# Kernel tuning notes

Hardware: AMD Instinct MI355X
Metric: run time of the kernel (lower is better)

Reference implementation:

```python
import jax, jax.numpy as jnp
import numpy as np

H, W, NUM_HEADS = 32, 32, 8


def dwconv3x3(x, w, b):
    # x: (B,C,H,W), w: (C,1,3,3) depthwise, b: (C,)
    y = jax.lax.conv_general_dilated(
        x, w, window_strides=(1, 1), padding='SAME',
        dimension_numbers=('NCHW', 'OIHW', 'NCHW'),
        feature_group_count=x.shape[1])
    return y + b[None, :, None, None]


def conv1x1(x, w, b):
    # x: (B,C,H,W), w: (O,C), b: (O,)
    return jnp.einsum('oc,bchw->bohw', w, x) + b[None, :, None, None]


def layernorm(x, w, b, eps=1e-6):
    mu = x.mean(-1, keepdims=True)
    var = ((x - mu) ** 2).mean(-1, keepdims=True)
    return (x - mu) / jnp.sqrt(var + eps) * w + b


def setup_inputs() -> dict:
    key = jax.random.key(0)
    ks = jax.random.split(key, 12)
    B, N, C = 32, H * W, 512
    Ch = 4 * C  # inverted MLP hidden
    s_lin = 0.02
    s_dw = np.sqrt(2.0 / 9.0)   # fan_out init for 3x3 depthwise
    s_pw1 = np.sqrt(2.0 / Ch)
    s_pw2 = np.sqrt(2.0 / C)
    return {
        'x': jax.random.normal(ks[0], (B, N, C), jnp.float32),
        'cpe_w': jax.random.normal(ks[1], (C, 1, 3, 3), jnp.float32) * s_dw,
        'cpe_b': jnp.zeros((C,), jnp.float32),
        'ln1_w': jnp.ones((C,), jnp.float32),
        'ln1_b': jnp.zeros((C,), jnp.float32),
        'qkv_w': jax.random.normal(ks[2], (3 * C, C), jnp.float32) * s_lin,
        'crpe_w': jax.random.normal(ks[3], (C, 1, 3, 3), jnp.float32) * s_dw,
        'crpe_b': jnp.zeros((C,), jnp.float32),
        'ln2_w': jnp.ones((C,), jnp.float32),
        'ln2_b': jnp.zeros((C,), jnp.float32),
        'fc1_w': jax.random.normal(ks[4], (Ch, C), jnp.float32) * s_pw1,
        'fc1_b': jnp.zeros((Ch,), jnp.float32),
        'dw_w': jax.random.normal(ks[5], (Ch, 1, 3, 3), jnp.float32) * s_dw,
        'dw_b': jnp.zeros((Ch,), jnp.float32),
        'fc2_w': jax.random.normal(ks[6], (C, Ch), jnp.float32) * s_pw2,
        'fc2_b': jnp.zeros((C,), jnp.float32),
    }


def reference(x, cpe_w, cpe_b, ln1_w, ln1_b, qkv_w, crpe_w, crpe_b,
              ln2_w, ln2_b, fc1_w, fc1_b, dw_w, dw_b, fc2_w, fc2_b):
    B, N, C = x.shape
    h = NUM_HEADS
    d = C // h
    scale = d ** -0.5

    # --- Convolutional position encoding: x = x + dwconv(x) ---
    img = x.reshape(B, H, W, C).transpose(0, 3, 1, 2)  # B C H W
    img = img + dwconv3x3(img, cpe_w, cpe_b)
    x = img.transpose(0, 2, 3, 1).reshape(B, N, C)

    # --- Factorized attention + conv relative position encoding ---
    cur = layernorm(x, ln1_w, ln1_b)
    qkv = cur @ qkv_w.T                                 # (B,N,3C)
    qkv = qkv.reshape(B, N, 3, h, d).transpose(2, 0, 3, 1, 4)  # (3,B,h,N,d)
    q, k, v = qkv[0], qkv[1], qkv[2]
    k_softmax = jax.nn.softmax(k, axis=2)               # softmax over tokens N
    ktv = jnp.einsum('bhnk,bhnv->bhkv', k_softmax, v)   # (B,h,d,d)
    factor_att = jnp.einsum('bhnk,bhkv->bhnv', q, ktv)  # (B,h,N,d)
    # crpe: depthwise conv on v as image, elementwise-multiplied by q
    v_img = v.transpose(0, 1, 3, 2).reshape(B, h * d, H, W)
    v_img = dwconv3x3(v_img, crpe_w, crpe_b)
    v_conv = v_img.reshape(B, h, d, N).transpose(0, 1, 3, 2)
    crpe = q * v_conv
    attn_out = (scale * factor_att + crpe).transpose(0, 2, 1, 3).reshape(B, N, C)
    x = x + attn_out

    # --- Inverted MLP (conv-based channel mixing) ---
    cur = layernorm(x, ln2_w, ln2_b)
    img = cur.reshape(B, H, W, C).transpose(0, 3, 1, 2)  # B C H W
    hdn = conv1x1(img, fc1_w, fc1_b)
    hdn = jax.nn.gelu(hdn, approximate=False)
    hdn = hdn + dwconv3x3(hdn, dw_w, dw_b)
    out = conv1x1(hdn, fc2_w, fc2_b)
    x = x + out.transpose(0, 2, 3, 1).reshape(B, N, C)
    return x
```

## Files before the change

### kernel.cpp

```cpp
#include <hip/hip_runtime.h>
#include <hip/hip_bf16.h>

using bf16 = __hip_bfloat16;
using s16x4 = __attribute__((ext_vector_type(4))) short;
using s16x8 = __attribute__((ext_vector_type(8))) short;
using f32x4 = __attribute__((ext_vector_type(4))) float;

#define DI __device__ __forceinline__

template <int N> DI void wvm() {
    if constexpr (N == 8) asm volatile("s_waitcnt vmcnt(8)" ::: "memory");
    else if constexpr (N == 4) asm volatile("s_waitcnt vmcnt(4)" ::: "memory");
    else if constexpr (N == 2) asm volatile("s_waitcnt vmcnt(2)" ::: "memory");
    else asm volatile("s_waitcnt vmcnt(0)" ::: "memory");
}

DI float b2f(short s) { union { unsigned u; float f; } z; z.u = ((unsigned)(unsigned short)s) << 16; return z.f; }
DI short f2b(float f) { bf16 t = __float2bfloat16(f); return *(short*)&t; }

DI float gelu_f(float x) {
    const float t = 0.7978845608f * x * (1.f + 0.044715f * x * x);
    const float e = __expf(2.f * t);
    const float th = 1.f - 2.f / (e + 1.f);
    return 0.5f * x * (1.f + th);
}

DI void ld8(const bf16* p, float* f) {
    s16x8 x = *(const s16x8*)(const void*)p;
#pragma unroll
    for (int c = 0; c < 8; c++) f[c] = b2f(x[c]);
}
DI void ld8(const float* p, float* f) {
    float4 a = *(const float4*)p, b = *(const float4*)(p + 4);
    f[0]=a.x; f[1]=a.y; f[2]=a.z; f[3]=a.w; f[4]=b.x; f[5]=b.y; f[6]=b.z; f[7]=b.w;
}

typedef const __attribute__((address_space(1))) void* gp_t;
typedef __attribute__((address_space(3))) void* lp_t;
DI void gload_lds16(const void* g, void* l) {
    __builtin_amdgcn_global_load_lds((gp_t)g, (lp_t)l, 16, 0, 0);
}

__global__ void diag_k(float* out, float v) { out[0] = v; }

__global__ void f2bf_k(const float* __restrict__ in, bf16* __restrict__ out, int n) {
    int i = (blockIdx.x * 256 + threadIdx.x) * 8;
    if (i >= n) return;
    float f[8];
    ld8(in + i, f);
    s16x8 o;
#pragma unroll
    for (int c = 0; c < 8; c++) o[c] = f2b(f[c]);
    *(s16x8*)(void*)(out + i) = o;
}

DI void tap10(const float* r, float w0, float w1, float w2, float* acc) {
#pragma unroll
    for (int i = 0; i < 8; i++)
        acc[i] += w0 * r[i] + w1 * r[i + 1] + w2 * r[i + 2];
}

template <typename TI, typename TO, bool RESID, int CPL>
__global__ __launch_bounds__(256) void conv4_k(
    const TI* in, long rs, long coff,
    const float* __restrict__ w, const float* __restrict__ bias,
    TO* out, long ors, int gshift)
{
    constexpr int CH = 64 * CPL;
    constexpr int ECNT = CH / 8;
    __shared__ float buf[2][CH][33];
    const int t = threadIdx.x;
    const int band = blockIdx.x & 3;
    const int cg = (blockIdx.x >> 2) & ((1 << gshift) - 1);
    const int img = blockIdx.x >> (2 + gshift);
    const int y0 = band * 8;

    const int spx = t >> 3;
    const int sce = (t & 7) * ECNT;
    const TI* gsrc = in + ((long)img << 10) * rs + coff + (long)cg * CH + sce;

    const int c = t & 63;
    const int xb = (t >> 6) * 8;

    float wv9[9][CPL], bw[CPL];
#pragma unroll
    for (int p = 0; p < CPL; p++) {
        const int gch = cg * CH + c * CPL + p;
#pragma unroll
        for (int j = 0; j < 9; j++) wv9[j][p] = w[gch * 9 + j];
        bw[p] = bias[gch];
    }

    auto stage = [&](int row) {
        float f[ECNT];
        ld8(gsrc + (long)(row * 32 + spx) * rs, f);
        if constexpr (ECNT == 16) ld8(gsrc + (long)(row * 32 + spx) * rs + 8, f + 8);
        float* d = &buf[row & 1][0][0];
#pragma unroll
        for (int k = 0; k < ECNT; k++) {
            const int ch = sce + k;
            const int rr = (CPL == 2) ? ((ch & 1) * 64 + (ch >> 1)) : ch;
            d[rr * 33 + spx] = f[k];
        }
    };
    auto slice = [&](int row, float r[CPL][10]) {
#pragma unroll
        for (int p = 0; p < CPL; p++) {
            const float* s = &buf[row & 1][c + p * 64][0];
            r[p][0] = (xb == 0) ? 0.f : s[xb - 1];
#pragma unroll
            for (int i = 0; i < 8; i++) r[p][1 + i] = s[xb + i];
            r[p][9] = (xb + 8 >= 32) ? 0.f : s[xb + 8];
        }
    };
    auto zero = [&](float r[CPL][10]) {
#pragma unroll
        for (int p = 0; p < CPL; p++)
#pragma unroll
            for (int i = 0; i < 10; i++) r[p][i] = 0.f;
    };

    float r0[CPL][10], r1[CPL][10], r2[CPL][10];
    if (y0 > 0) stage(y0 - 1);
    __syncthreads();
    if (y0 > 0) slice(y0 - 1, r0); else zero(r0);
    stage(y0);
    __syncthreads();
    slice(y0, r1);

    for (int y = y0; y < y0 + 8; ++y) {
        const int yn = y + 1;
        if (yn <= 31) stage(yn);
        __syncthreads();
        if (yn <= 31) slice(yn, r2); else zero(r2);
        float acc[CPL][8];
#pragma unroll
        for (int p = 0; p < CPL; p++) {
#pragma unroll
            for (int i = 0; i < 8; i++) acc[p][i] = bw[p];
            tap10(r0[p], wv9[0][p], wv9[1][p], wv9[2][p], acc[p]);
            tap10(r1[p], wv9[3][p], wv9[4][p], wv9[5][p], acc[p]);
            tap10(r2[p], wv9[6][p], wv9[7][p], wv9[8][p], acc[p]);
            if (RESID) {
#pragma unroll
                for (int i = 0; i < 8; i++) acc[p][i] += r1[p][i + 1];
            }
        }
        TO* o = out + ((long)(img * 1024 + y * 32 + xb)) * ors + (long)cg * CH + c * CPL;
#pragma unroll
        for (int i = 0; i < 8; i++) {
            if constexpr (CPL == 2 && sizeof(TO) == 2) {
                const unsigned u = (unsigned)(unsigned short)f2b(acc[0][i]) |
                                   ((unsigned)(unsigned short)f2b(acc[1][i]) << 16);
                *(unsigned*)(void*)(o + (long)i * ors) = u;
            } else {
                o[(long)i * ors] = (TO)acc[0][i];
            }
        }
#pragma unroll
        for (int p = 0; p < CPL; p++)
#pragma unroll
            for (int i = 0; i < 10; i++) { r0[p][i] = r1[p][i]; r1[p][i] = r2[p][i]; }
    }
}

__global__ __launch_bounds__(256) void ln_k(const float* __restrict__ x,
                                            const float* __restrict__ w,
                                            const float* __restrict__ bp,
                                            bf16* __restrict__ out)
{
    const size_t row = blockIdx.x * 4 + (threadIdx.x >> 6);
    const int t = threadIdx.x & 63;
    const float* xr = x + row * 512;
    alignas(16) float v[8];
    *(float4*)&v[0] = *(const float4*)(xr + t * 8);
    *(float4*)&v[4] = *(const float4*)(xr + t * 8 + 4);
    float s = 0.f;
#pragma unroll
    for (int j = 0; j < 8; j++) s += v[j];
#pragma unroll
    for (int mm = 32; mm; mm >>= 1) s += __shfl_xor(s, mm);
    const float mu = s * (1.f / 512.f);
    float q = 0.f;
#pragma unroll
    for (int j = 0; j < 8; j++) { v[j] -= mu; q += v[j] * v[j]; }
#pragma unroll
    for (int mm = 32; mm; mm >>= 1) q += __shfl_xor(q, mm);
    const float rstd = rsqrtf(q * (1.f / 512.f) + 1e-6f);
    alignas(16) float wv[8], bv[8];
    *(float4*)&wv[0] = *(const float4*)(w + t * 8);
    *(float4*)&wv[4] = *(const float4*)(w + t * 8 + 4);
    *(float4*)&bv[0] = *(const float4*)(bp + t * 8);
    *(float4*)&bv[4] = *(const float4*)(bp + t * 8 + 4);
    alignas(16) bf16 o[8];
#pragma unroll
    for (int j = 0; j < 8; j++) o[j] = __float2bfloat16(v[j] * rstd * wv[j] + bv[j]);
    *(uint4*)(out + row * 512 + t * 8) = *(const uint4*)o;
}

template <int EPI, int K, int NY, bool DUAL = false>
__global__ __launch_bounds__(512) void gemm8p_k(
    const bf16* __restrict__ A, const bf16* __restrict__ A2,
    const bf16* __restrict__ Bw, const float* __restrict__ bias,
    const float* resid, bf16* __restrict__ outb, float* outf, int M, int Nn)
{
    constexpr int KT = K / 64;
    constexpr int LDA = DUAL ? K / 2 : K;
    __shared__ __align__(16) char lds[131072];
    char* ldsA = lds;
    char* ldsB = lds + 65536;
    const int t = threadIdx.x;
    const int lane = t & 63;
    const int w = t >> 6;
    const int wr = w >> 2, wc = w & 3;
    const int nwg = 128 * NY;
    const int swz = (blockIdx.x & 7) * (nwg >> 3) + (blockIdx.x >> 3);
    const int m0 = (swz / NY) * 256;
    const int n0 = (swz % NY) * 256;
    const int lr = lane & 15, lg = lane >> 4;

    f32x4 acc[8][4] = {};

    const int srow = lane >> 3;
    const int ssrc = 8 * ((lane & 7) ^ srow);

    auto SA = [&](int b, int kt, int h) {
        const bf16* Ab = A;
        int ktl = kt;
        if constexpr (DUAL) { if (kt >= KT / 2) { Ab = A2; ktl = kt - KT / 2; } }
#pragma unroll
        for (int j = 0; j < 2; j++) {
            const int lrow0 = j * 64 + w * 8;
            const int R0 = j * 128 + h * 64 + (lrow0 & 63);
            gload_lds16(Ab + (size_t)(m0 + R0 + srow) * LDA + ktl * 64 + ssrc,
                        ldsA + ((b * 2 + h) * 128 + lrow0) * 128);
        }
    };
    auto SB = [&](int b, int kt, int h) {
#pragma unroll
        for (int j = 0; j < 2; j++) {
            const int lrow0 = j * 64 + w * 8;
            const int R0 = (lrow0 >> 5) * 64 + h * 32 + (lrow0 & 31);
            gload_lds16(Bw + (size_t)(n0 + R0 + srow) * K + kt * 64 + ssrc,
                        ldsB + ((b * 2 + h) * 128 + lrow0) * 128);
        }
    };
    auto RA = [&](int b, int h, int m, int ks) -> s16x8 {
        return *(const s16x8*)(ldsA + ((b * 2 + h) * 128 + wr * 64 + m * 16 + lr) * 128
                               + (((ks * 4 + lg) ^ (lr & 7)) << 4));
    };
    auto RB = [&](int b, int h, int n, int ks) -> s16x8 {
        return *(const s16x8*)(ldsB + ((b * 2 + h) * 128 + wc * 32 + n * 16 + lr) * 128
                               + (((ks * 4 + lg) ^ (lr & 7)) << 4));
    };
    auto MM = [&](int mb, int nb, s16x8 (&a)[2][4], s16x8 (&b)[2][2]) {
#pragma unroll
        for (int ks = 0; ks < 2; ks++)
#pragma unroll
            for (int m = 0; m < 4; m++)
#pragma unroll
                for (int n = 0; n < 2; n++)
                    acc[mb + m][nb + n] =
                        __builtin_amdgcn_mfma_f32_16x16x32_bf16(a[ks][m], b[ks][n], acc[mb + m][nb + n], 0, 0, 0);
    };

    SA(0, 0, 0); SB(0, 0, 0); SA(0, 0, 1); SB(0, 0, 1);
    SA(1, 1, 0); SB(1, 1, 0);
    wvm<8>();
    __builtin_amdgcn_s_barrier();

    s16x8 aLo[2][4], aHi[2][4], bLo[2][2], bHi[2][2];
    auto TILE = [&](int kt) {
        const int b = kt & 1;
#pragma unroll
        for (int ks = 0; ks < 2; ks++) {
#pragma unroll
            for (int m = 0; m < 4; m++) aLo[ks][m] = RA(b, 0, m, ks);
#pragma unroll
            for (int n = 0; n < 2; n++) bLo[ks][n] = RB(b, 0, n, ks);
        }
        if (kt + 1 < KT) SA(b ^ 1, kt + 1, 1);
        __builtin_amdgcn_s_barrier();
        __builtin_amdgcn_s_setprio(1);
        MM(0, 0, aLo, bLo);
        __builtin_amdgcn_s_setprio(0);
        if (kt + 1 < KT) wvm<8>(); else wvm<2>();
        __builtin_amdgcn_s_barrier();
#pragma unroll
        for (int ks = 0; ks < 2; ks++)
#pragma unroll
            for (int m = 0; m < 4; m++) aHi[ks][m] = RA(b, 1, m, ks);
        if (kt + 1 < KT) SB(b ^ 1, kt + 1, 1);
        __builtin_amdgcn_s_barrier();
        __builtin_amdgcn_s_setprio(1);
        MM(4, 0, aHi, bLo);
        __builtin_amdgcn_s_setprio(0);
        if (kt + 1 < KT) wvm<8>(); else wvm<0>();
        __builtin_amdgcn_s_barrier();
#pragma unroll
        for (int ks = 0; ks < 2; ks++)
#pragma unroll
            for (int n = 0; n < 2; n++) bHi[ks][n] = RB(b, 1, n, ks);
        if (kt + 2 < KT) SA(b, kt + 2, 0);
        __builtin_amdgcn_s_barrier();
        __builtin_amdgcn_s_setprio(1);
        MM(4, 2, aHi, bHi);
        __builtin_amdgcn_s_setprio(0);
        __builtin_amdgcn_s_barrier();
        if (kt + 2 < KT) SB(b, kt + 2, 0);
        __builtin_amdgcn_s_barrier();
        __builtin_amdgcn_s_setprio(1);
        MM(0, 2, aLo, bHi);
        __builtin_amdgcn_s_setprio(0);
        if (kt + 2 < KT) { wvm<8>(); __builtin_amdgcn_s_barrier(); }
        else if (kt + 1 < KT) { wvm<4>(); __builtin_amdgcn_s_barrier(); }
    };

    if constexpr (KT <= 8) {
#pragma unroll
        for (int kt = 0; kt < KT; ++kt) TILE(kt);
    } else {
#pragma unroll 2
        for (int kt = 0; kt < KT; ++kt) TILE(kt);
    }

#pragma unroll
    for (int i = 0; i < 8; i++) {
#pragma unroll
        for (int j = 0; j < 4; j++) {
            const int col = n0 + wc * 64 + j * 16 + lr;
            float bcol = 0.f;
            if constexpr (EPI >= 1) bcol = bias[col];
#pragma unroll
            for (int r = 0; r < 4; r++) {
                const int row = m0 + wr * 128 + i * 16 + lg * 4 + r;
                float v = acc[i][j][r] + bcol;
                const size_t idx = (size_t)row * Nn + col;
                if (EPI == 2) outf[idx] = v + resid[idx];
                else outb[idx] = __float2bfloat16(EPI == 1 ? gelu_f(v) : v);
            }
        }
    }
}

__global__ __launch_bounds__(256) void ktv2_k(const bf16* __restrict__ qkv,
                                              bf16* __restrict__ ktvT)
{
    __shared__ __align__(16) char P[64 * 128];
    __shared__ __align__(16) char Vt[64 * 128];
    __shared__ float csl[64 * 5];
    const int t = threadIdx.x;
    const int b = blockIdx.x >> 3, hh = blockIdx.x & 7;
    const int lane = t & 63, w = t >> 6;
    const int lr = lane & 15, lg = lane >> 4;

    const int n_r = t >> 2;
    const int k0 = (t & 3) * 16;
    const bf16* kbase = qkv + (size_t)(b * 1024) * 1536 + 512 + hh * 64 + k0;
    const bf16* vbase = kbase + 512;

    const int kq = t & 63, qq = t >> 6;
    float cacc = 0.f;

    f32x4 acc[4] = {};

    for (int n0 = 0; n0 < 1024; n0 += 64) {
        const uint4 ka = *(const uint4*)(kbase + (size_t)(n0 + n_r) * 1536);
        const uint4 kb2 = *(const uint4*)(kbase + (size_t)(n0 + n_r) * 1536 + 8);
        const uint4 va = *(const uint4*)(vbase + (size_t)(n0 + n_r) * 1536);
        const uint4 vb2 = *(const uint4*)(vbase + (size_t)(n0 + n_r) * 1536 + 8);
        __syncthreads();
        {
            const short* ke = (const short*)&ka;
            const short* ke2 = (const short*)&kb2;
            const short* ve = (const short*)&va;
            const short* ve2 = (const short*)&vb2;
            const int nslot = ((n_r >> 3) << 4);
            const int nbyte = (n_r & 7) * 2;
#pragma unroll
            for (int j = 0; j < 16; j++) {
                const int row = k0 + j;
                const short kv = j < 8 ? ke[j] : ke2[j - 8];
                const short vv = j < 8 ? ve[j] : ve2[j - 8];
                const int off = row * 128 + (nslot ^ ((row & 7) << 4)) + nbyte;
                *(short*)(P + off) = f2b(__expf(b2f(kv)));
                *(short*)(Vt + off) = vv;
            }
        }
        __syncthreads();
        {
            const char* pr = P + kq * 128;
            const int sw = (kq & 7) << 4;
            s16x8 x0 = *(const s16x8*)(pr + (((qq * 2) << 4) ^ sw));
            s16x8 x1 = *(const s16x8*)(pr + (((qq * 2 + 1) << 4) ^ sw));
#pragma unroll
            for (int j = 0; j < 8; j++) cacc += b2f(x0[j]) + b2f(x1[j]);
        }
#pragma unroll
        for (int ks2 = 0; ks2 < 2; ks2++) {
            s16x8 aF = *(const s16x8*)(Vt + (w * 16 + lr) * 128 + (((ks2 * 4 + lg) ^ (lr & 7)) << 4));
            s16x8 bF[4];
#pragma unroll
            for (int j = 0; j < 4; j++)
                bF[j] = *(const s16x8*)(P + (j * 16 + lr) * 128 + (((ks2 * 4 + lg) ^ (lr & 7)) << 4));
#pragma unroll
            for (int j = 0; j < 4; j++)
                acc[j] = __builtin_amdgcn_mfma_f32_16x16x32_bf16(aF, bF[j], acc[j], 0, 0, 0);
        }
    }
    __syncthreads();
    csl[kq * 5 + qq] = cacc;
    __syncthreads();
    if (t < 64) csl[t * 5 + 4] = csl[t * 5] + csl[t * 5 + 1] + csl[t * 5 + 2] + csl[t * 5 + 3];
    __syncthreads();

    bf16* o = ktvT + (size_t)(b * 8 + hh) * 4096;
#pragma unroll
    for (int j = 0; j < 4; j++) {
        const int col = j * 16 + lr;
        const float sc = 0.125f / csl[col * 5 + 4];
#pragma unroll
        for (int r = 0; r < 4; r++) {
            const int vrow = w * 16 + lg * 4 + r;
            o[vrow * 64 + col] = __float2bfloat16(acc[j][r] * sc);
        }
    }
}

__global__ __launch_bounds__(256) void attnout2_k(
    float* xs, const bf16* __restrict__ qkv,
    const bf16* __restrict__ ktvT, const bf16* __restrict__ vc)
{
    __shared__ __align__(16) char qs[256 * 128];
    __shared__ __align__(16) char ks[64 * 128];
    const int t = threadIdx.x;
    const int bid = blockIdx.x;
    const int b = bid >> 5, hh = (bid >> 2) & 7, nc = bid & 3;
    const int n0 = nc * 256;
    const int lane = t & 63, w = t >> 6;
    const int lr = lane & 15, lg = lane >> 4;

    {
        const int r0 = t >> 3, sl = t & 7;
#pragma unroll
        for (int it = 0; it < 8; it++) {
            const int row = it * 32 + r0;
            const uint4 v = *(const uint4*)(qkv + ((size_t)(b * 1024 + n0 + row)) * 1536 + hh * 64 + sl * 8);
            *(uint4*)(qs + row * 128 + ((sl ^ (row & 7)) << 4)) = v;
        }
#pragma unroll
        for (int it = 0; it < 2; it++) {
            const int u = it * 256 + t;
            const int vr = u >> 3, sl2 = u & 7;
            const uint4 vv = *(const uint4*)(ktvT + (size_t)(b * 8 + hh) * 4096 + vr * 64 + sl2 * 8);
            *(uint4*)(ks + vr * 128 + ((sl2 ^ (vr & 7)) << 4)) = vv;
        }
    }
    __syncthreads();

    f32x4 acc[4][4] = {};
    s16x8 aF[2][4], bF[2][4];
#pragma unroll
    for (int ksi = 0; ksi < 2; ksi++) {
#pragma unroll
        for (int m = 0; m < 4; m++) {
            const int row = w * 64 + m * 16 + lr;
            aF[ksi][m] = *(const s16x8*)(qs + row * 128 + (((ksi * 4 + lg) ^ (lr & 7)) << 4));
        }
#pragma unroll
        for (int j = 0; j < 4; j++) {
            const int vr = j * 16 + lr;
            bF[ksi][j] = *(const s16x8*)(ks + vr * 128 + (((ksi * 4 + lg) ^ (lr & 7)) << 4));
        }
    }
#pragma unroll
    for (int ksi = 0; ksi < 2; ksi++)
#pragma unroll
        for (int m = 0; m < 4; m++)
#pragma unroll
            for (int j = 0; j < 4; j++)
                acc[m][j] = __builtin_amdgcn_mfma_f32_16x16x32_bf16(aF[ksi][m], bF[ksi][j], acc[m][j], 0, 0, 0);

#pragma unroll
    for (int m = 0; m < 4; m++) {
#pragma unroll
        for (int j = 0; j < 4; j++) {
#pragma unroll
            for (int r = 0; r < 4; r++) {
                const int lrow = w * 64 + m * 16 + lg * 4 + r;
                const int col = j * 16 + lr;
                const size_t idx = ((size_t)(b * 1024 + n0 + lrow)) * 512 + hh * 64 + col;
                const short qv = *(const short*)(qs + lrow * 128 + ((((col >> 3) ^ (lrow & 7)) << 4)) + (col & 7) * 2);
                xs[idx] = xs[idx] + acc[m][j][r] + b2f(qv) * __bfloat162float(vc[idx]);
            }
        }
    }
}

static constexpr size_t OFF_WQ   = 0;
static constexpr size_t OFF_W1   = 1572864;
static constexpr size_t OFF_W2   = 3670016;
static constexpr size_t OFF_CUR  = 5767168;
static constexpr size_t OFF_H2B  = 5767168;
static constexpr size_t OFF_QKV  = 72876032;
static constexpr size_t OFF_HG   = 72876032;
static constexpr size_t OFF_VC   = 173539328;
static constexpr size_t OFF_H2A  = 139984896;
static constexpr size_t OFF_KTV  = 207093760;
static constexpr size_t WS_NEED  = 207618048;

extern "C" void kernel_launch(void* const* d_in, const int* in_sizes, int n_in,
                              void* d_out, int out_size, void* d_ws, size_t ws_size,
                              hipStream_t stream)
{
    const float* x     = (const float*)d_in[0];
    const float* cpe_w = (const float*)d_in[1];
    const float* cpe_b = (const float*)d_in[2];
    const float* ln1_w = (const float*)d_in[3];
    const float* ln1_b = (const float*)d_in[4];
    const float* qkv_w = (const float*)d_in[5];
    const float* crpe_w= (const float*)d_in[6];
    const float* crpe_b= (const float*)d_in[7];
    const float* ln2_w = (const float*)d_in[8];
    const float* ln2_b = (const float*)d_in[9];
    const float* fc1_w = (const float*)d_in[10];
    const float* fc1_b = (const float*)d_in[11];
    const float* dw_w  = (const float*)d_in[12];
    const float* dw_b  = (const float*)d_in[13];
    const float* fc2_w = (const float*)d_in[14];
    const float* fc2_b = (const float*)d_in[15];
    float* spine = (float*)d_out;
    char* ws = (char*)d_ws;

    if (ws_size < WS_NEED) {
        diag_k<<<1, 1, 0, stream>>>(spine, (float)ws_size);
        return;
    }

    bf16*  wq   = (bf16*)(ws + OFF_WQ);
    bf16*  w1   = (bf16*)(ws + OFF_W1);
    bf16*  w2b  = (bf16*)(ws + OFF_W2);
    bf16*  cur  = (bf16*)(ws + OFF_CUR);
    bf16*  qkv  = (bf16*)(ws + OFF_QKV);
    bf16*  vc   = (bf16*)(ws + OFF_VC);
    bf16*  ktvT = (bf16*)(ws + OFF_KTV);
    bf16*  hg   = (bf16*)(ws + OFF_HG);
    bf16*  h2a  = (bf16*)(ws + OFF_H2A);
    bf16*  h2b  = (bf16*)(ws + OFF_H2B);

    f2bf_k<<<(1536 * 512 / 8 + 255) / 256, 256, 0, stream>>>(qkv_w, wq, 1536 * 512);
    f2bf_k<<<(2048 * 512 / 8 + 255) / 256, 256, 0, stream>>>(fc1_w, w1, 2048 * 512);
    f2bf_k<<<(2048 * 512 / 8 + 255) / 256, 256, 0, stream>>>(fc2_w, w2b, 512 * 2048);

    conv4_k<float, float, true, 1><<<32 * 8 * 4, 256, 0, stream>>>(x, 512, 0, cpe_w, cpe_b, spine, 512, 3);

    const int M = 32768;
    ln_k<<<M / 4, 256, 0, stream>>>(spine, ln1_w, ln1_b, cur);
    gemm8p_k<0, 512, 6><<<768, 512, 0, stream>>>(cur, nullptr, wq, nullptr, nullptr, qkv, nullptr, M, 1536);
    ktv2_k<<<256, 256, 0, stream>>>(qkv, ktvT);
    conv4_k<bf16, bf16, false, 2><<<32 * 4 * 4, 256, 0, stream>>>(qkv, 1536, 1024, crpe_w, crpe_b, vc, 512, 2);
    attnout2_k<<<32 * 8 * 4, 256, 0, stream>>>(spine, qkv, ktvT, vc);
    ln_k<<<M / 4, 256, 0, stream>>>(spine, ln2_w, ln2_b, cur);

    gemm8p_k<1, 512, 4><<<512, 512, 0, stream>>>(cur, nullptr, w1, fc1_b, nullptr, hg, nullptr, M, 1024);
    conv4_k<bf16, bf16, true, 2><<<32 * 8 * 4, 256, 0, stream>>>(hg, 1024, 0, dw_w, dw_b, h2a, 1024, 3);
    gemm8p_k<1, 512, 4><<<512, 512, 0, stream>>>(cur, nullptr, w1 + (size_t)1024 * 512, fc1_b + 1024, nullptr, hg, nullptr, M, 1024);
    conv4_k<bf16, bf16, true, 2><<<32 * 8 * 4, 256, 0, stream>>>(hg, 1024, 0, dw_w + (size_t)1024 * 9, dw_b + 1024, h2b, 1024, 3);
    gemm8p_k<2, 2048, 2, true><<<256, 512, 0, stream>>>(h2a, h2b, w2b, fc2_b, spine, nullptr, spine, M, 512);
}
```

Measured before the change: 478.3 us.

## Replace fc2 GEMM with dedicated 128x256-tile double-buffered kernel

The fc2 projection (K=2048, N=512) no longer uses the generic 256x256 eight-wave GEMM with a DUAL A-source mode. It now runs in a new kernel with 4 waves, 128x256 tiles, a 32-wide K step and simple double-buffered LDS staging. This doubles the number of workgroups from 256 to 512 to fill more of the GPU's compute units for this narrow-N GEMM. In exchange, each tile reuses data less and synchronises more often (a full vmcnt wait and barrier every K step), and the generic kernel loses its DUAL path.

```diff
diff --git a/kernel.cpp b/kernel.cpp
--- a/kernel.cpp
+++ b/kernel.cpp
@@ -198,14 +198,13 @@
     *(uint4*)(out + row * 512 + t * 8) = *(const uint4*)o;
 }
 
-template <int EPI, int K, int NY, bool DUAL = false>
+template <int EPI, int K, int NY>
 __global__ __launch_bounds__(512) void gemm8p_k(
-    const bf16* __restrict__ A, const bf16* __restrict__ A2,
-    const bf16* __restrict__ Bw, const float* __restrict__ bias,
-    const float* resid, bf16* __restrict__ outb, float* outf, int M, int Nn)
+    const bf16* __restrict__ A, const bf16* __restrict__ Bw,
+    const float* __restrict__ bias, const float* resid,
+    bf16* __restrict__ outb, float* outf, int M, int Nn)
 {
     constexpr int KT = K / 64;
-    constexpr int LDA = DUAL ? K / 2 : K;
     __shared__ __align__(16) char lds[131072];
     char* ldsA = lds;
     char* ldsB = lds + 65536;
@@ -225,14 +224,11 @@
     const int ssrc = 8 * ((lane & 7) ^ srow);
 
     auto SA = [&](int b, int kt, int h) {
-        const bf16* Ab = A;
-        int ktl = kt;
-        if constexpr (DUAL) { if (kt >= KT / 2) { Ab = A2; ktl = kt - KT / 2; } }
 #pragma unroll
         for (int j = 0; j < 2; j++) {
             const int lrow0 = j * 64 + w * 8;
             const int R0 = j * 128 + h * 64 + (lrow0 & 63);
-            gload_lds16(Ab + (size_t)(m0 + R0 + srow) * LDA + ktl * 64 + ssrc,
+            gload_lds16(A + (size_t)(m0 + R0 + srow) * K + kt * 64 + ssrc,
                         ldsA + ((b * 2 + h) * 128 + lrow0) * 128);
         }
     };
@@ -316,13 +312,8 @@
         else if (kt + 1 < KT) { wvm<4>(); __builtin_amdgcn_s_barrier(); }
     };
 
-    if constexpr (KT <= 8) {
-#pragma unroll
-        for (int kt = 0; kt < KT; ++kt) TILE(kt);
-    } else {
-#pragma unroll 2
-        for (int kt = 0; kt < KT; ++kt) TILE(kt);
-    }
+#pragma unroll
+    for (int kt = 0; kt < KT; ++kt) TILE(kt);
 
 #pragma unroll
     for (int i = 0; i < 8; i++) {
@@ -338,6 +329,87 @@
                 const size_t idx = (size_t)row * Nn + col;
                 if (EPI == 2) outf[idx] = v + resid[idx];
                 else outb[idx] = __float2bfloat16(EPI == 1 ? gelu_f(v) : v);
+            }
+        }
+    }
+}
+
+__global__ __launch_bounds__(256) void gemmfc3_k(
+    const bf16* __restrict__ A, const bf16* __restrict__ A2,
+    const bf16* __restrict__ Bw, const float* __restrict__ bias,
+    const float* resid, float* outf, int M, int Nn)
+{
+    constexpr int KT = 64;
+    __shared__ __align__(16) short As[2][128 * 32];
+    __shared__ __align__(16) short Bs[2][256 * 32];
+    const int t = threadIdx.x;
+    const int lane = t & 63;
+    const int wv = t >> 6;
+    const int nwg = 512;
+    const int swz = (blockIdx.x & 7) * (nwg >> 3) + (blockIdx.x >> 3);
+    const int m0 = (swz >> 1) * 128;
+    const int n0 = (swz & 1) * 256;
+    const int lr = lane & 15, lg = lane >> 4;
+
+    f32x4 acc[8][4] = {};
+
+    const int srow = lane >> 2;
+    const int sk = 8 * ((lane & 3) ^ ((lane >> 3) & 3));
+    const int rsw = (lr >> 1) & 3;
+
+    auto STAGE = [&](int buf, int kt) {
+        const bf16* Ab = (kt < 32) ? A : A2;
+        const int kc = ((kt < 32) ? kt : kt - 32) * 32 + sk;
+#pragma unroll
+        for (int j = 0; j < 2; j++) {
+            const int r = wv * 32 + j * 16 + srow;
+            gload_lds16(Ab + (size_t)(m0 + r) * 1024 + kc,
+                        (char*)&As[buf][0] + (wv * 32 + j * 16) * 64);
+        }
+#pragma unroll
+        for (int j = 0; j < 4; j++) {
+            const int r = wv * 64 + j * 16 + srow;
+            gload_lds16(Bw + (size_t)(n0 + r) * 2048 + kt * 32 + sk,
+                        (char*)&Bs[buf][0] + (wv * 64 + j * 16) * 64);
+        }
+    };
+
+    auto COMPUTE = [&](int buf) {
+        s16x8 aF[8], bF[4];
+#pragma unroll
+        for (int i = 0; i < 8; i++)
+            aF[i] = *(const s16x8*)((const char*)&As[buf][0] + (i * 16 + lr) * 64 + ((lg ^ rsw) << 4));
+#pragma unroll
+        for (int j = 0; j < 4; j++)
+            bF[j] = *(const s16x8*)((const char*)&Bs[buf][0] + (wv * 64 + j * 16 + lr) * 64 + ((lg ^ rsw) << 4));
+#pragma unroll
+        for (int i = 0; i < 8; i++)
+#pragma unroll
+            for (int j = 0; j < 4; j++)
+                acc[i][j] = __builtin_amdgcn_mfma_f32_16x16x32_bf16(aF[i], bF[j], acc[i][j], 0, 0, 0);
+    };
+
+    STAGE(0, 0);
+    wvm<0>();
+    __builtin_amdgcn_s_barrier();
+    for (int kt = 0; kt < KT; ++kt) {
+        if (kt + 1 < KT) STAGE((kt + 1) & 1, kt + 1);
+        COMPUTE(kt & 1);
+        wvm<0>();
+        __builtin_amdgcn_s_barrier();
+    }
+
+#pragma unroll
+    for (int i = 0; i < 8; i++) {
+#pragma unroll
+        for (int j = 0; j < 4; j++) {
+            const int col = n0 + wv * 64 + j * 16 + lr;
+            const float bcol = bias[col];
+#pragma unroll
+            for (int r = 0; r < 4; r++) {
+                const int row = m0 + i * 16 + lg * 4 + r;
+                const size_t idx = (size_t)row * Nn + col;
+                outf[idx] = acc[i][j][r] + bcol + resid[idx];
             }
         }
     }
@@ -556,15 +628,15 @@
 
     const int M = 32768;
     ln_k<<<M / 4, 256, 0, stream>>>(spine, ln1_w, ln1_b, cur);
-    gemm8p_k<0, 512, 6><<<768, 512, 0, stream>>>(cur, nullptr, wq, nullptr, nullptr, qkv, nullptr, M, 1536);
+    gemm8p_k<0, 512, 6><<<768, 512, 0, stream>>>(cur, wq, nullptr, nullptr, qkv, nullptr, M, 1536);
     ktv2_k<<<256, 256, 0, stream>>>(qkv, ktvT);
     conv4_k<bf16, bf16, false, 2><<<32 * 4 * 4, 256, 0, stream>>>(qkv, 1536, 1024, crpe_w, crpe_b, vc, 512, 2);
     attnout2_k<<<32 * 8 * 4, 256, 0, stream>>>(spine, qkv, ktvT, vc);
     ln_k<<<M / 4, 256, 0, stream>>>(spine, ln2_w, ln2_b, cur);
 
-    gemm8p_k<1, 512, 4><<<512, 512, 0, stream>>>(cur, nullptr, w1, fc1_b, nullptr, hg, nullptr, M, 1024);
+    gemm8p_k<1, 512, 4><<<512, 512, 0, stream>>>(cur, w1, fc1_b, nullptr, hg, nullptr, M, 1024);
     conv4_k<bf16, bf16, true, 2><<<32 * 8 * 4, 256, 0, stream>>>(hg, 1024, 0, dw_w, dw_b, h2a, 1024, 3);
-    gemm8p_k<1, 512, 4><<<512, 512, 0, stream>>>(cur, nullptr, w1 + (size_t)1024 * 512, fc1_b + 1024, nullptr, hg, nullptr, M, 1024);
+    gemm8p_k<1, 512, 4><<<512, 512, 0, stream>>>(cur, w1 + (size_t)1024 * 512, fc1_b + 1024, nullptr, hg, nullptr, M, 1024);
     conv4_k<bf16, bf16, true, 2><<<32 * 8 * 4, 256, 0, stream>>>(hg, 1024, 0, dw_w + (size_t)1024 * 9, dw_b + 1024, h2b, 1024, 3);
-    gemm8p_k<2, 2048, 2, true><<<256, 512, 0, stream>>>(h2a, h2b, w2b, fc2_b, spine, nullptr, spine, M, 512);
-}
+    gemmfc3_k<<<512, 256, 0, stream>>>(h2a, h2b, w2b, fc2_b, spine, spine, M, 512);
+}
```

New measurement: 525.3 us. 9.8% more time.
